# Kernel tuning notes

Hardware: AMD Instinct MI355X
Metric: run time of the kernel (lower is better)

The kernel has to match this reference:

```python
import jax, jax.numpy as jnp
import numpy as np

N = 100000      # num nodes
E = 3200000     # num edges
F = 128         # feature dim (in == out, required by final in-place copy)
U = 1000        # num_users


def gcn_conv(x, edge_index, W, b):
    """PyG GCNConv: symmetric-normalized adjacency with self-loops.
    out = D^{-1/2} (A + I) D^{-1/2} X W + b
    """
    xw = x @ W                                   # [N, F]
    src, dst = edge_index[0], edge_index[1]
    # in-degree including the self-loop (+1)
    deg = jax.ops.segment_sum(jnp.ones((E,), x.dtype), dst, num_segments=N) + 1.0
    inv_sqrt = jax.lax.rsqrt(deg)                # [N]
    coef = inv_sqrt[src] * inv_sqrt[dst]         # [E]
    agg = jax.ops.segment_sum(xw[src] * coef[:, None], dst, num_segments=N)
    # self-loop contribution: norm_ii = inv_sqrt[i]^2
    return agg + xw * (inv_sqrt * inv_sqrt)[:, None] + b


def setup_inputs() -> dict:
    key = jax.random.key(0)
    k1, k2, k3, k4, k5, k6 = jax.random.split(key, 6)
    x = jax.random.normal(k1, (N, F), dtype=jnp.float32)
    edge_index = jax.random.randint(k2, (2, E), 0, N, dtype=jnp.int64)
    s = 1.0 / np.sqrt(F)
    W1 = jax.random.normal(k3, (F, F), dtype=jnp.float32) * s
    b1 = jnp.zeros((F,), dtype=jnp.float32)
    W2 = jax.random.normal(k4, (F, F), dtype=jnp.float32) * s
    b2 = jnp.zeros((F,), dtype=jnp.float32)
    return {"x": x, "edge_index": edge_index, "W1": W1, "b1": b1, "W2": W2, "b2": b2}


def reference(x, edge_index, W1, b1, W2, b2):
    # eval mode: dropout(p=0.5, training=False) is identity; detach is a no-op in fwd
    h = jax.nn.elu(gcn_conv(x, edge_index, W1, b1))
    h = jax.nn.elu(gcn_conv(h, edge_index, W2, b2))
    # x[num_users:] = movie_features  -> movie rows restored to original input
    return jnp.concatenate([h[:U], x[U:]], axis=0)
```

## Files before the change

### kernel.cpp

```cpp
#include <hip/hip_runtime.h>


#define F_DIM 128
#define U_USERS 1000
#define SCAN_CHUNK 1024
#define NFCAP 48000
#define NCHUNK 3
#define SBIN 40960
#define SW (SBIN / 2)
#define PSLICE 85
#define XPAD 136
#define BMW 3136
#define SMEM_BYTES (128 * XPAD * 2 + 64 * XPAD * 2)

using f16x8 = __attribute__((ext_vector_type(8))) _Float16;
using f16x2 = __attribute__((ext_vector_type(2))) _Float16;
using f32x4 = __attribute__((ext_vector_type(4))) float;

union H4 { uint2 u2; _Float16 h[4]; };

__global__ __launch_bounds__(1024) void hist_kernel(const int* __restrict__ src,
                                                    const int* __restrict__ dst,
                                                    unsigned int* __restrict__ partial,
                                                    int* __restrict__ fr, int E, int n) {
    __shared__ unsigned int h[SW];
    int tid = threadIdx.x;
    int c = blockIdx.x % NCHUNK;
    int p = blockIdx.x / NCHUNK;
    for (int i = tid; i < SW; i += 1024) h[i] = 0u;
    __syncthreads();

    int lo = c * SBIN;
    int hi = lo + SBIN;
    int len = (E + PSLICE - 1) / PSLICE;
    int base = p * len;
    int end = min(E, base + len);
    int e = base + tid * 4;
    for (; e + 3 < end; e += 4096) {
        int4 dv = *(const int4*)(dst + e);
#pragma unroll
        for (int i = 0; i < 4; ++i) {
            int d = ((const int*)&dv)[i];
            if ((unsigned)d < (unsigned)n) {
                if (d >= lo && d < hi) {
                    int local = d - lo;
                    atomicAdd(&h[local >> 1], 1u << ((local & 1) << 4));
                }
                if (c == 0 && d < U_USERS) {
                    int s = src[e + i];
                    if ((unsigned)s < (unsigned)n) fr[s] = 1;
                }
            }
        }
    }
    for (; e < end; ++e) {
        int d = dst[e];
        if ((unsigned)d < (unsigned)n) {
            if (d >= lo && d < hi) {
                int local = d - lo;
                atomicAdd(&h[local >> 1], 1u << ((local & 1) << 4));
            }
            if (c == 0 && d < U_USERS) {
                int s = src[e];
                if ((unsigned)s < (unsigned)n) fr[s] = 1;
            }
        }
    }
    __syncthreads();
    unsigned int* outp = partial + ((size_t)(c * PSLICE + p)) * SW;
    for (int i = tid; i < SW; i += 1024) outp[i] = h[i];
}

__global__ void reduce_prep_kernel(const unsigned int* __restrict__ partial,
                                   float* __restrict__ inv, int* __restrict__ fr,
                                   int* __restrict__ degF,
                                   unsigned int* __restrict__ bitsG, int n) {
    int t = blockIdx.x * blockDim.x + threadIdx.x;
    if (t >= NCHUNK * SW) return;
    int c = t / SW, w = t % SW;
    unsigned int a0 = 0, a1 = 0;
    const unsigned int* basep = partial + (size_t)c * PSLICE * SW + w;
#pragma unroll 5
    for (int p = 0; p < PSLICE; ++p) {
        unsigned int v = basep[(size_t)p * SW];
        a0 += v & 0xFFFFu;
        a1 += v >> 16;
    }
    int i0 = c * SBIN + 2 * w;
    unsigned int pair = 0u;
#pragma unroll
    for (int k = 0; k < 2; ++k) {
        int i = i0 + k;
        unsigned int dg = k ? a1 : a0;
        if (i < n) {
            inv[i] = rsqrtf((float)dg + 1.0f);
            bool isfr = (i < U_USERS) || (fr[i] != 0);
            if (i < U_USERS) fr[i] = 1;
            degF[i] = isfr ? (int)dg : 0;
            if (isfr) pair |= (1u << k);
        }
    }
    if (pair) atomicOr(&bitsG[i0 >> 5], pair << (i0 & 31));
}

__global__ void scan_reduce2_kernel(const int* __restrict__ dA, const int* __restrict__ dB,
                                    int* __restrict__ pA, int* __restrict__ pB, int n) {
    __shared__ int sdata[256];
    int b = blockIdx.x, t = threadIdx.x;
    int base = b * SCAN_CHUNK;
    int sumA = 0, sumB = 0;
#pragma unroll
    for (int i = 0; i < 4; ++i) {
        int idx = base + t + 256 * i;
        if (idx < n) { sumA += dA[idx]; sumB += dB[idx]; }
    }
    sdata[t] = sumA; __syncthreads();
    for (int s = 128; s > 0; s >>= 1) { if (t < s) sdata[t] += sdata[t + s]; __syncthreads(); }
    if (t == 0) pA[b] = sdata[0];
    __syncthreads();
    sdata[t] = sumB; __syncthreads();
    for (int s = 128; s > 0; s >>= 1) { if (t < s) sdata[t] += sdata[t + s]; __syncthreads(); }
    if (t == 0) pB[b] = sdata[0];
}

__global__ void scan_partials2_kernel(int* __restrict__ pA, int* __restrict__ pB, int nb) {
    int wv = threadIdx.x >> 6, lane = threadIdx.x & 63;
    int* p = wv ? pB : pA;
    int i0 = lane * 2, i1 = lane * 2 + 1;
    int v0 = (i0 < nb) ? p[i0] : 0;
    int v1 = (i1 < nb) ? p[i1] : 0;
    int sum = v0 + v1;
    int incl = sum;
    for (int ofs = 1; ofs < 64; ofs <<= 1) {
        int t = __shfl_up(incl, ofs);
        if (lane >= ofs) incl += t;
    }
    int run = incl - sum;
    if (i0 < nb) p[i0] = run;
    if (i1 < nb) p[i1] = run + v0;
}

__global__ void scan_final2_kernel(const int* __restrict__ dA, const int* __restrict__ pA,
                                   int* __restrict__ rp,
                                   const int* __restrict__ dB, const int* __restrict__ pB,
                                   int* __restrict__ remap,
                                   int* __restrict__ flist, int* __restrict__ nf_dev, int n) {
    __shared__ int sthread[256];
    int b = blockIdx.x, t = threadIdx.x;
    int base = b * SCAN_CHUNK;
    {
        int v[4]; int sum = 0;
#pragma unroll
        for (int i = 0; i < 4; ++i) { int idx = base + 4 * t + i; v[i] = (idx < n) ? dA[idx] : 0; sum += v[i]; }
        sthread[t] = sum; __syncthreads();
        for (int ofs = 1; ofs < 256; ofs <<= 1) {
            int val = (t >= ofs) ? sthread[t - ofs] : 0;
            __syncthreads(); sthread[t] += val; __syncthreads();
        }
        int run = sthread[t] - sum + pA[b];
#pragma unroll
        for (int i = 0; i < 4; ++i) { int idx = base + 4 * t + i; if (idx < n) rp[idx] = run; run += v[i]; }
        __syncthreads();
    }
    {
        int v[4]; int sum = 0;
#pragma unroll
        for (int i = 0; i < 4; ++i) { int idx = base + 4 * t + i; v[i] = (idx < n) ? dB[idx] : 0; sum += v[i]; }
        sthread[t] = sum; __syncthreads();
        for (int ofs = 1; ofs < 256; ofs <<= 1) {
            int val = (t >= ofs) ? sthread[t - ofs] : 0;
            __syncthreads(); sthread[t] += val; __syncthreads();
        }
        int run = sthread[t] - sum + pB[b];
#pragma unroll
        for (int i = 0; i < 4; ++i) {
            int idx = base + 4 * t + i;
            if (idx < n) {
                remap[idx] = run;
                if (v[i] && run < NFCAP) flist[run] = idx;
                if (idx == n - 1) *nf_dev = min(run + v[i], NFCAP);
            }
            run += v[i];
        }
    }
}

__device__ __forceinline__ void fill_csr_body(const int* __restrict__ src,
                                              const int* __restrict__ dst,
                                              const unsigned int* __restrict__ bitsG,
                                              int* __restrict__ rp, int* __restrict__ col,
                                              int E, int n, int fblk,
                                              unsigned char* smem) {
    unsigned int* bm = (unsigned int*)smem;
    int tid = threadIdx.x;
    int nw = (n + 31) >> 5;
    for (int i = tid; i < nw; i += 256) bm[i] = bitsG[i];
    __syncthreads();

    int t = fblk * 256 + tid;
    int e0 = t * 4;
    if (e0 + 3 < E) {
        int4 dv = *(const int4*)(dst + e0);
        int4 sv = *(const int4*)(src + e0);
        const int* dp = (const int*)&dv;
        const int* sp = (const int*)&sv;
        bool f[4];
#pragma unroll
        for (int i = 0; i < 4; ++i) {
            int d = dp[i];
            f[i] = ((unsigned)d < (unsigned)n) && ((unsigned)sp[i] < (unsigned)n)
                   && ((bm[d >> 5] >> (d & 31)) & 1u);
        }
        int pos[4];
#pragma unroll
        for (int i = 0; i < 4; ++i) {
            pos[i] = -1;
            if (f[i]) pos[i] = atomicAdd(&rp[dp[i]], 1);
        }
#pragma unroll
        for (int i = 0; i < 4; ++i) {
            if (f[i] && (unsigned)pos[i] < (unsigned)E) col[pos[i]] = sp[i];
        }
    } else {
        for (int e = e0; e < E; ++e) {
            int d = dst[e], s = src[e];
            if ((unsigned)d < (unsigned)n && (unsigned)s < (unsigned)n &&
                ((bm[d >> 5] >> (d & 31)) & 1u)) {
                int pos = atomicAdd(&rp[d], 1);
                if ((unsigned)pos < (unsigned)E) col[pos] = s;
            }
        }
    }
}

__device__ __forceinline__ void gemm_mfma_body(const float* __restrict__ X,
                                               const float* __restrict__ W,
                                               _Float16* __restrict__ outh,
                                               float* __restrict__ pout,
                                               int nrows, int rowBase,
                                               unsigned char* smem) {
    _Float16* Wt = (_Float16*)smem;
    _Float16* Xs = Wt + 128 * XPAD;

    int tid = threadIdx.x;

    const float4* W4 = (const float4*)W;
#pragma unroll
    for (int i = 0; i < 16; ++i) {
        int j = tid + 256 * i;
        int k = j >> 5;
        int n4 = j & 31;
        float4 v = W4[j];
#pragma unroll
        for (int q = 0; q < 4; ++q)
            Wt[(n4 * 4 + q) * XPAD + k] = (_Float16)((const float*)&v)[q];
    }

#pragma unroll
    for (int i = 0; i < 8; ++i) {
        int j = tid + 256 * i;
        int r = j >> 5;
        int k4 = j & 31;
        int row = rowBase + r;
        float4 v = make_float4(0.f, 0.f, 0.f, 0.f);
        if (row < nrows) {
            v = ((const float4*)(X + (size_t)row * F_DIM))[k4];
            if (pout != nullptr && row >= U_USERS)
                ((float4*)(pout + (size_t)row * F_DIM))[k4] = v;
        }
        H4 p;
#pragma unroll
        for (int q = 0; q < 4; ++q) p.h[q] = (_Float16)((const float*)&v)[q];
        *(uint2*)&Xs[r * XPAD + k4 * 4] = p.u2;
    }
    __syncthreads();

    int w = tid >> 6;
    int lane = tid & 63;
    int m = lane & 15;
    int quad = lane >> 4;
    int R = w * 16;

    f32x4 acc[8];
#pragma unroll
    for (int i = 0; i < 8; ++i) acc[i] = (f32x4){0.f, 0.f, 0.f, 0.f};

#pragma unroll
    for (int kc = 0; kc < 4; ++kc) {
        f16x8 a = *(const f16x8*)&Xs[(R + m) * XPAD + kc * 32 + quad * 8];
#pragma unroll
        for (int ct = 0; ct < 8; ++ct) {
            f16x8 b = *(const f16x8*)&Wt[(ct * 16 + m) * XPAD + kc * 32 + quad * 8];
            acc[ct] = __builtin_amdgcn_mfma_f32_16x16x32_f16(a, b, acc[ct], 0, 0, 0);
        }
    }

#pragma unroll
    for (int ct = 0; ct < 8; ++ct) {
#pragma unroll
        for (int reg = 0; reg < 4; ++reg) {
            int row = rowBase + R + quad * 4 + reg;
            if (row < nrows)
                outh[(size_t)row * F_DIM + ct * 16 + m] = (_Float16)acc[ct][reg];
        }
    }
}

__global__ __launch_bounds__(256) void gemm_fill_kernel(const float* __restrict__ X,
                                                        const float* __restrict__ W,
                                                        _Float16* __restrict__ outh,
                                                        float* __restrict__ pout, int nrows,
                                                        int gemmBlocks,
                                                        const int* __restrict__ src,
                                                        const int* __restrict__ dst,
                                                        const unsigned int* __restrict__ bitsG,
                                                        int* __restrict__ rp,
                                                        int* __restrict__ col, int E, int n) {
    __shared__ __align__(16) unsigned char smem[SMEM_BYTES];
    int b = blockIdx.x;
    if (b < gemmBlocks) {
        gemm_mfma_body(X, W, outh, pout, nrows, b * 64, smem);
    } else {
        fill_csr_body(src, dst, bitsG, rp, col, E, n, b - gemmBlocks, smem);
    }
}

__global__ __launch_bounds__(256) void gemm_f16_dyn_kernel(const float* __restrict__ X,
                                                           const float* __restrict__ W,
                                                           _Float16* __restrict__ outh,
                                                           const int* __restrict__ nrows_p) {
    __shared__ __align__(16) unsigned char smem[SMEM_BYTES];
    int nrows = *nrows_p;
    int rowBase = blockIdx.x * 64;
    if (rowBase >= nrows) return;
    gemm_mfma_body(X, W, outh, nullptr, nrows, rowBase, smem);
}

__global__ __launch_bounds__(256) void gather_l1_kernel(const _Float16* __restrict__ xwh,
                                                        const float* __restrict__ inv,
                                                        const int* __restrict__ rp,
                                                        const int* __restrict__ col,
                                                        const int* __restrict__ flist,
                                                        const int* __restrict__ nf_p,
                                                        const float* __restrict__ b,
                                                        float* __restrict__ h1c) {
    int ci = blockIdx.x * 4 + (threadIdx.x >> 6);
    if (ci >= *nf_p) return;
    int lane = threadIdx.x & 63;
    int node = flist[ci];
    int start = (node == 0) ? 0 : rp[node - 1];
    int end = rp[node];

    float accx = 0.f, accy = 0.f;
    for (int base = start; base < end; base += 64) {
        int j = base + lane;
        int s_l = 0; float c_l = 0.f;
        if (j < end) { s_l = col[j]; c_l = inv[s_l]; }
        int cnt = min(64, end - base);
        int i = 0;
        for (; i + 4 <= cnt; i += 4) {
            int s0 = __shfl(s_l, i + 0); float f0 = __shfl(c_l, i + 0);
            int s1 = __shfl(s_l, i + 1); float f1 = __shfl(c_l, i + 1);
            int s2 = __shfl(s_l, i + 2); float f2 = __shfl(c_l, i + 2);
            int s3 = __shfl(s_l, i + 3); float f3 = __shfl(c_l, i + 3);
            f16x2 v0 = ((const f16x2*)(xwh + (size_t)s0 * F_DIM))[lane];
            f16x2 v1 = ((const f16x2*)(xwh + (size_t)s1 * F_DIM))[lane];
            f16x2 v2 = ((const f16x2*)(xwh + (size_t)s2 * F_DIM))[lane];
            f16x2 v3 = ((const f16x2*)(xwh + (size_t)s3 * F_DIM))[lane];
            accx += (float)v0[0] * f0 + (float)v1[0] * f1 + (float)v2[0] * f2 + (float)v3[0] * f3;
            accy += (float)v0[1] * f0 + (float)v1[1] * f1 + (float)v2[1] * f2 + (float)v3[1] * f3;
        }
        for (; i < cnt; ++i) {
            int s0 = __shfl(s_l, i); float f0 = __shfl(c_l, i);
            f16x2 v0 = ((const f16x2*)(xwh + (size_t)s0 * F_DIM))[lane];
            accx += (float)v0[0] * f0;
            accy += (float)v0[1] * f0;
        }
    }

    float ivd = inv[node];
    f16x2 self = ((const f16x2*)(xwh + (size_t)node * F_DIM))[lane];
    float vx = accx * ivd + (float)self[0] * ivd * ivd + b[lane * 2];
    float vy = accy * ivd + (float)self[1] * ivd * ivd + b[lane * 2 + 1];
    vx = vx > 0.f ? vx : expf(vx) - 1.f;
    vy = vy > 0.f ? vy : expf(vy) - 1.f;
    ((float2*)(h1c + (size_t)ci * F_DIM))[lane] = make_float2(vx, vy);
}

__global__ __launch_bounds__(256) void gather_l2_kernel(const _Float16* __restrict__ xwc,
                                                        const float* __restrict__ inv,
                                                        const int* __restrict__ rp,
                                                        const int* __restrict__ col,
                                                        const int* __restrict__ remap,
                                                        const float* __restrict__ b,
                                                        float* __restrict__ out) {
    int node = blockIdx.x * 4 + (threadIdx.x >> 6);
    if (node >= U_USERS) return;
    int lane = threadIdx.x & 63;
    int start = (node == 0) ? 0 : rp[node - 1];
    int end = rp[node];

    float accx = 0.f, accy = 0.f;
    for (int base = start; base < end; base += 64) {
        int j = base + lane;
        int r_l = 0; float c_l = 0.f;
        if (j < end) { int s = col[j]; c_l = inv[s]; r_l = remap[s]; }
        int cnt = min(64, end - base);
        int i = 0;
        for (; i + 4 <= cnt; i += 4) {
            int r0 = __shfl(r_l, i + 0); float f0 = __shfl(c_l, i + 0);
            int r1 = __shfl(r_l, i + 1); float f1 = __shfl(c_l, i + 1);
            int r2 = __shfl(r_l, i + 2); float f2 = __shfl(c_l, i + 2);
            int r3 = __shfl(r_l, i + 3); float f3 = __shfl(c_l, i + 3);
            f16x2 v0 = ((const f16x2*)(xwc + (size_t)r0 * F_DIM))[lane];
            f16x2 v1 = ((const f16x2*)(xwc + (size_t)r1 * F_DIM))[lane];
            f16x2 v2 = ((const f16x2*)(xwc + (size_t)r2 * F_DIM))[lane];
            f16x2 v3 = ((const f16x2*)(xwc + (size_t)r3 * F_DIM))[lane];
            accx += (float)v0[0] * f0 + (float)v1[0] * f1 + (float)v2[0] * f2 + (float)v3[0] * f3;
            accy += (float)v0[1] * f0 + (float)v1[1] * f1 + (float)v2[1] * f2 + (float)v3[1] * f3;
        }
        for (; i < cnt; ++i) {
            int rr = __shfl(r_l, i); float f0 = __shfl(c_l, i);
            f16x2 v0 = ((const f16x2*)(xwc + (size_t)rr * F_DIM))[lane];
            accx += (float)v0[0] * f0;
            accy += (float)v0[1] * f0;
        }
    }

    float ivd = inv[node];
    f16x2 self = ((const f16x2*)(xwc + (size_t)node * F_DIM))[lane];
    float vx = accx * ivd + (float)self[0] * ivd * ivd + b[lane * 2];
    float vy = accy * ivd + (float)self[1] * ivd * ivd + b[lane * 2 + 1];
    vx = vx > 0.f ? vx : expf(vx) - 1.f;
    vy = vy > 0.f ? vy : expf(vy) - 1.f;
    ((float2*)(out + (size_t)node * F_DIM))[lane] = make_float2(vx, vy);
}

extern "C" void kernel_launch(void* const* d_in, const int* in_sizes, int n_in,
                              void* d_out, int out_size, void* d_ws, size_t ws_size,
                              hipStream_t stream) {
    const float* x  = (const float*)d_in[0];
    const int*   ei = (const int*)d_in[1];
    const float* W1 = (const float*)d_in[2];
    const float* b1 = (const float*)d_in[3];
    const float* W2 = (const float*)d_in[4];
    const float* b2 = (const float*)d_in[5];
    float* out = (float*)d_out;

    int n = in_sizes[0] / F_DIM;
    int E = in_sizes[1] / 2;
    const int* srcI = ei;
    const int* dstI = ei + E;

    _Float16* xwh = (_Float16*)d_ws;
    float* h1c   = (float*)(xwh + (size_t)n * F_DIM);
    float* inv   = h1c + (size_t)NFCAP * F_DIM;
    int* fr      = (int*)(inv + n);
    int* degF    = fr + n;
    int* remap   = degF + n;
    int* rp      = remap + n;
    int* flist   = rp + n;
    int* pA      = flist + NFCAP;
    int* pB      = pA + 1024;
    int* nf_dev  = pB + 1024;
    int* col     = nf_dev + 16;
    unsigned int* partialH = (unsigned int*)(col + E);
    unsigned int* bitsG = partialH + (size_t)NCHUNK * PSLICE * SW;

    int nb = (n + SCAN_CHUNK - 1) / SCAN_CHUNK;

    hipMemsetAsync(fr, 0, (size_t)n * sizeof(int), stream);
    hipMemsetAsync(bitsG, 0, (size_t)BMW * sizeof(unsigned int), stream);

    hist_kernel<<<NCHUNK * PSLICE, 1024, 0, stream>>>(srcI, dstI, partialH, fr, E, n);
    reduce_prep_kernel<<<(NCHUNK * SW + 255) / 256, 256, 0, stream>>>(partialH, inv, fr, degF, bitsG, n);

    scan_reduce2_kernel<<<nb, 256, 0, stream>>>(degF, fr, pA, pB, n);
    scan_partials2_kernel<<<1, 128, 0, stream>>>(pA, pB, nb);
    scan_final2_kernel<<<nb, 256, 0, stream>>>(degF, pA, rp, fr, pB, remap, flist, nf_dev, n);

    int gemmBlocks = (n + 63) / 64;
    int fillBlocks = (E / 4 + 255) / 256;
    gemm_fill_kernel<<<gemmBlocks + fillBlocks, 256, 0, stream>>>(
        x, W1, xwh, out, n, gemmBlocks, srcI, dstI, bitsG, rp, col, E, n);

    gather_l1_kernel<<<(NFCAP + 3) / 4, 256, 0, stream>>>(xwh, inv, rp, col, flist, nf_dev, b1, h1c);

    gemm_f16_dyn_kernel<<<(NFCAP + 63) / 64, 256, 0, stream>>>(h1c, W2, xwh, nf_dev);
    gather_l2_kernel<<<(U_USERS + 3) / 4, 256, 0, stream>>>(xwh, inv, rp, col, remap, b2, out);
}
```

Baseline: 299.1 us.

## Pre-transpose weights to fp16 once and read B fragments from global

Adds a small kernel that converts and transposes W1 and W2 to fp16 once per call. The GEMM bodies then load MFMA B operands directly from global/L2 instead of each block staging a transposed W copy in LDS, which removes the per-block W conversion and shrinks shared memory to the X tile, allowing higher occupancy. The fused kernel also reorders blocks so the CSR fill blocks are dispatched before the GEMM blocks. The cost is one extra launch, and B reads now come from cache rather than LDS with less reuse per block.

```diff
diff --git a/kernel.cpp b/kernel.cpp
--- a/kernel.cpp
+++ b/kernel.cpp
@@ -11,13 +11,24 @@
 #define PSLICE 85
 #define XPAD 136
 #define BMW 3136
-#define SMEM_BYTES (128 * XPAD * 2 + 64 * XPAD * 2)
+#define SMEM_BYTES (64 * XPAD * 2)
 
 using f16x8 = __attribute__((ext_vector_type(8))) _Float16;
 using f16x2 = __attribute__((ext_vector_type(2))) _Float16;
 using f32x4 = __attribute__((ext_vector_type(4))) float;
 
 union H4 { uint2 u2; _Float16 h[4]; };
+
+__global__ __launch_bounds__(128) void wprep_kernel(const float* __restrict__ W1,
+                                                    const float* __restrict__ W2,
+                                                    _Float16* __restrict__ wt1,
+                                                    _Float16* __restrict__ wt2) {
+    int nr = blockIdx.x & 127;
+    const float* W = (blockIdx.x < 128) ? W1 : W2;
+    _Float16* o = (blockIdx.x < 128) ? wt1 : wt2;
+    int k = threadIdx.x;
+    o[nr * 128 + k] = (_Float16)W[k * 128 + nr];
+}
 
 __global__ __launch_bounds__(1024) void hist_kernel(const int* __restrict__ src,
                                                     const int* __restrict__ dst,
@@ -234,27 +245,13 @@
 }
 
 __device__ __forceinline__ void gemm_mfma_body(const float* __restrict__ X,
-                                               const float* __restrict__ W,
+                                               const _Float16* __restrict__ wth,
                                                _Float16* __restrict__ outh,
                                                float* __restrict__ pout,
                                                int nrows, int rowBase,
                                                unsigned char* smem) {
-    _Float16* Wt = (_Float16*)smem;
-    _Float16* Xs = Wt + 128 * XPAD;
-
+    _Float16* Xs = (_Float16*)smem;
     int tid = threadIdx.x;
-
-    const float4* W4 = (const float4*)W;
-#pragma unroll
-    for (int i = 0; i < 16; ++i) {
-        int j = tid + 256 * i;
-        int k = j >> 5;
-        int n4 = j & 31;
-        float4 v = W4[j];
-#pragma unroll
-        for (int q = 0; q < 4; ++q)
-            Wt[(n4 * 4 + q) * XPAD + k] = (_Float16)((const float*)&v)[q];
-    }
 
 #pragma unroll
     for (int i = 0; i < 8; ++i) {
@@ -290,7 +287,7 @@
         f16x8 a = *(const f16x8*)&Xs[(R + m) * XPAD + kc * 32 + quad * 8];
 #pragma unroll
         for (int ct = 0; ct < 8; ++ct) {
-            f16x8 b = *(const f16x8*)&Wt[(ct * 16 + m) * XPAD + kc * 32 + quad * 8];
+            f16x8 b = *(const f16x8*)&wth[(size_t)(ct * 16 + m) * F_DIM + kc * 32 + quad * 8];
             acc[ct] = __builtin_amdgcn_mfma_f32_16x16x32_f16(a, b, acc[ct], 0, 0, 0);
         }
     }
@@ -307,10 +304,10 @@
 }
 
 __global__ __launch_bounds__(256) void gemm_fill_kernel(const float* __restrict__ X,
-                                                        const float* __restrict__ W,
+                                                        const _Float16* __restrict__ wth,
                                                         _Float16* __restrict__ outh,
                                                         float* __restrict__ pout, int nrows,
-                                                        int gemmBlocks,
+                                                        int fillBlocks,
                                                         const int* __restrict__ src,
                                                         const int* __restrict__ dst,
                                                         const unsigned int* __restrict__ bitsG,
@@ -318,22 +315,22 @@
                                                         int* __restrict__ col, int E, int n) {
     __shared__ __align__(16) unsigned char smem[SMEM_BYTES];
     int b = blockIdx.x;
-    if (b < gemmBlocks) {
-        gemm_mfma_body(X, W, outh, pout, nrows, b * 64, smem);
+    if (b < fillBlocks) {
+        fill_csr_body(src, dst, bitsG, rp, col, E, n, b, smem);
     } else {
-        fill_csr_body(src, dst, bitsG, rp, col, E, n, b - gemmBlocks, smem);
+        gemm_mfma_body(X, wth, outh, pout, nrows, (b - fillBlocks) * 64, smem);
     }
 }
 
 __global__ __launch_bounds__(256) void gemm_f16_dyn_kernel(const float* __restrict__ X,
-                                                           const float* __restrict__ W,
+                                                           const _Float16* __restrict__ wth,
                                                            _Float16* __restrict__ outh,
                                                            const int* __restrict__ nrows_p) {
     __shared__ __align__(16) unsigned char smem[SMEM_BYTES];
     int nrows = *nrows_p;
     int rowBase = blockIdx.x * 64;
     if (rowBase >= nrows) return;
-    gemm_mfma_body(X, W, outh, nullptr, nrows, rowBase, smem);
+    gemm_mfma_body(X, wth, outh, nullptr, nrows, rowBase, smem);
 }
 
 __global__ __launch_bounds__(256) void gather_l1_kernel(const _Float16* __restrict__ xwh,
@@ -466,11 +463,15 @@
     int* col     = nf_dev + 16;
     unsigned int* partialH = (unsigned int*)(col + E);
     unsigned int* bitsG = partialH + (size_t)NCHUNK * PSLICE * SW;
+    _Float16* wt1h = (_Float16*)(bitsG + BMW);
+    _Float16* wt2h = wt1h + 16384;
 
     int nb = (n + SCAN_CHUNK - 1) / SCAN_CHUNK;
 
     hipMemsetAsync(fr, 0, (size_t)n * sizeof(int), stream);
     hipMemsetAsync(bitsG, 0, (size_t)BMW * sizeof(unsigned int), stream);
+
+    wprep_kernel<<<256, 128, 0, stream>>>(W1, W2, wt1h, wt2h);
 
     hist_kernel<<<NCHUNK * PSLICE, 1024, 0, stream>>>(srcI, dstI, partialH, fr, E, n);
     reduce_prep_kernel<<<(NCHUNK * SW + 255) / 256, 256, 0, stream>>>(partialH, inv, fr, degF, bitsG, n);
@@ -479,13 +480,13 @@
     scan_partials2_kernel<<<1, 128, 0, stream>>>(pA, pB, nb);
     scan_final2_kernel<<<nb, 256, 0, stream>>>(degF, pA, rp, fr, pB, remap, flist, nf_dev, n);
 
+    int fillBlocks = (E / 4 + 255) / 256;
     int gemmBlocks = (n + 63) / 64;
-    int fillBlocks = (E / 4 + 255) / 256;
-    gemm_fill_kernel<<<gemmBlocks + fillBlocks, 256, 0, stream>>>(
-        x, W1, xwh, out, n, gemmBlocks, srcI, dstI, bitsG, rp, col, E, n);
+    gemm_fill_kernel<<<fillBlocks + gemmBlocks, 256, 0, stream>>>(
+        x, wt1h, xwh, out, n, fillBlocks, srcI, dstI, bitsG, rp, col, E, n);
 
     gather_l1_kernel<<<(NFCAP + 3) / 4, 256, 0, stream>>>(xwh, inv, rp, col, flist, nf_dev, b1, h1c);
 
-    gemm_f16_dyn_kernel<<<(NFCAP + 63) / 64, 256, 0, stream>>>(h1c, W2, xwh, nf_dev);
+    gemm_f16_dyn_kernel<<<(NFCAP + 63) / 64, 256, 0, stream>>>(h1c, wt2h, xwh, nf_dev);
     gather_l2_kernel<<<(U_USERS + 3) / 4, 256, 0, stream>>>(xwh, inv, rp, col, remap, b2, out);
 }
```

After: 309.8 us. 1.04x slower.

## Load GEMM A operands straight to registers and swizzle W tile in LDS

Applied to the files above, without the earlier changes.

The MFMA GEMM no longer stages X rows through shared memory. Each lane loads its A fragments directly from global memory into registers and converts them to f16. The transposed W tile is stored unpadded with an XOR swizzle to avoid bank conflicts, which cuts LDS use to 32KB. The fused kernel also puts the fill-CSR blocks before the GEMM blocks so that the scatter work starts first. The trade-off is less coalesced global reads of X and strided per-element reads of W.

```diff
diff --git a/kernel.cpp b/kernel.cpp
--- a/kernel.cpp
+++ b/kernel.cpp
@@ -11,13 +11,11 @@
 #define PSLICE 85
 #define XPAD 136
 #define BMW 3136
-#define SMEM_BYTES (128 * XPAD * 2 + 64 * XPAD * 2)
+#define SMEM_BYTES 32768
 
 using f16x8 = __attribute__((ext_vector_type(8))) _Float16;
 using f16x2 = __attribute__((ext_vector_type(2))) _Float16;
 using f32x4 = __attribute__((ext_vector_type(4))) float;
-
-union H4 { uint2 u2; _Float16 h[4]; };
 
 __global__ __launch_bounds__(1024) void hist_kernel(const int* __restrict__ src,
                                                     const int* __restrict__ dst,
@@ -240,38 +238,18 @@
                                                int nrows, int rowBase,
                                                unsigned char* smem) {
     _Float16* Wt = (_Float16*)smem;
-    _Float16* Xs = Wt + 128 * XPAD;
-
     int tid = threadIdx.x;
-
-    const float4* W4 = (const float4*)W;
-#pragma unroll
-    for (int i = 0; i < 16; ++i) {
-        int j = tid + 256 * i;
-        int k = j >> 5;
-        int n4 = j & 31;
-        float4 v = W4[j];
-#pragma unroll
-        for (int q = 0; q < 4; ++q)
-            Wt[(n4 * 4 + q) * XPAD + k] = (_Float16)((const float*)&v)[q];
-    }
 
 #pragma unroll
     for (int i = 0; i < 8; ++i) {
         int j = tid + 256 * i;
-        int r = j >> 5;
-        int k4 = j & 31;
-        int row = rowBase + r;
-        float4 v = make_float4(0.f, 0.f, 0.f, 0.f);
-        if (row < nrows) {
-            v = ((const float4*)(X + (size_t)row * F_DIM))[k4];
-            if (pout != nullptr && row >= U_USERS)
-                ((float4*)(pout + (size_t)row * F_DIM))[k4] = v;
-        }
-        H4 p;
-#pragma unroll
-        for (int q = 0; q < 4; ++q) p.h[q] = (_Float16)((const float*)&v)[q];
-        *(uint2*)&Xs[r * XPAD + k4 * 4] = p.u2;
+        int nr = j & 127;
+        int k8 = j >> 7;
+        f16x8 v;
+#pragma unroll
+        for (int kk = 0; kk < 8; ++kk)
+            v[kk] = (_Float16)W[(k8 * 8 + kk) * F_DIM + nr];
+        *(f16x8*)&Wt[nr * F_DIM + ((k8 ^ (nr & 15)) * 8)] = v;
     }
     __syncthreads();
 
@@ -279,7 +257,35 @@
     int lane = tid & 63;
     int m = lane & 15;
     int quad = lane >> 4;
-    int R = w * 16;
+    int row = rowBase + w * 16 + m;
+    bool rv = row < nrows;
+
+    f16x8 a0, a1, a2, a3;
+    {
+        const float* xr = X + (size_t)row * F_DIM;
+        float* pr = (pout != nullptr && rv && row >= U_USERS)
+                        ? pout + (size_t)row * F_DIM : nullptr;
+#pragma unroll
+        for (int kc = 0; kc < 4; ++kc) {
+            float4 lo = make_float4(0.f, 0.f, 0.f, 0.f);
+            float4 hi = lo;
+            if (rv) {
+                lo = ((const float4*)(xr + kc * 32 + quad * 8))[0];
+                hi = ((const float4*)(xr + kc * 32 + quad * 8))[1];
+            }
+            if (pr) {
+                ((float4*)(pr + kc * 32 + quad * 8))[0] = lo;
+                ((float4*)(pr + kc * 32 + quad * 8))[1] = hi;
+            }
+            f16x8 av;
+            av[0] = (_Float16)lo.x; av[1] = (_Float16)lo.y;
+            av[2] = (_Float16)lo.z; av[3] = (_Float16)lo.w;
+            av[4] = (_Float16)hi.x; av[5] = (_Float16)hi.y;
+            av[6] = (_Float16)hi.z; av[7] = (_Float16)hi.w;
+            if (kc == 0) a0 = av; else if (kc == 1) a1 = av;
+            else if (kc == 2) a2 = av; else a3 = av;
+        }
+    }
 
     f32x4 acc[8];
 #pragma unroll
@@ -287,10 +293,11 @@
 
 #pragma unroll
     for (int kc = 0; kc < 4; ++kc) {
-        f16x8 a = *(const f16x8*)&Xs[(R + m) * XPAD + kc * 32 + quad * 8];
+        f16x8 a = (kc == 0) ? a0 : (kc == 1) ? a1 : (kc == 2) ? a2 : a3;
 #pragma unroll
         for (int ct = 0; ct < 8; ++ct) {
-            f16x8 b = *(const f16x8*)&Wt[(ct * 16 + m) * XPAD + kc * 32 + quad * 8];
+            f16x8 b = *(const f16x8*)&Wt[(ct * 16 + m) * F_DIM +
+                                         (((kc * 4 + quad) ^ m) * 8)];
             acc[ct] = __builtin_amdgcn_mfma_f32_16x16x32_f16(a, b, acc[ct], 0, 0, 0);
         }
     }
@@ -299,9 +306,9 @@
     for (int ct = 0; ct < 8; ++ct) {
 #pragma unroll
         for (int reg = 0; reg < 4; ++reg) {
-            int row = rowBase + R + quad * 4 + reg;
-            if (row < nrows)
-                outh[(size_t)row * F_DIM + ct * 16 + m] = (_Float16)acc[ct][reg];
+            int r = rowBase + w * 16 + quad * 4 + reg;
+            if (r < nrows)
+                outh[(size_t)r * F_DIM + ct * 16 + m] = (_Float16)acc[ct][reg];
         }
     }
 }
@@ -310,7 +317,7 @@
                                                         const float* __restrict__ W,
                                                         _Float16* __restrict__ outh,
                                                         float* __restrict__ pout, int nrows,
-                                                        int gemmBlocks,
+                                                        int fillBlocks,
                                                         const int* __restrict__ src,
                                                         const int* __restrict__ dst,
                                                         const unsigned int* __restrict__ bitsG,
@@ -318,10 +325,10 @@
                                                         int* __restrict__ col, int E, int n) {
     __shared__ __align__(16) unsigned char smem[SMEM_BYTES];
     int b = blockIdx.x;
-    if (b < gemmBlocks) {
-        gemm_mfma_body(X, W, outh, pout, nrows, b * 64, smem);
+    if (b < fillBlocks) {
+        fill_csr_body(src, dst, bitsG, rp, col, E, n, b, smem);
     } else {
-        fill_csr_body(src, dst, bitsG, rp, col, E, n, b - gemmBlocks, smem);
+        gemm_mfma_body(X, W, outh, pout, nrows, (b - fillBlocks) * 64, smem);
     }
 }
 
@@ -479,10 +486,10 @@
     scan_partials2_kernel<<<1, 128, 0, stream>>>(pA, pB, nb);
     scan_final2_kernel<<<nb, 256, 0, stream>>>(degF, pA, rp, fr, pB, remap, flist, nf_dev, n);
 
+    int fillBlocks = (E / 4 + 255) / 256;
     int gemmBlocks = (n + 63) / 64;
-    int fillBlocks = (E / 4 + 255) / 256;
-    gemm_fill_kernel<<<gemmBlocks + fillBlocks, 256, 0, stream>>>(
-        x, W1, xwh, out, n, gemmBlocks, srcI, dstI, bitsG, rp, col, E, n);
+    gemm_fill_kernel<<<fillBlocks + gemmBlocks, 256, 0, stream>>>(
+        x, W1, xwh, out, n, fillBlocks, srcI, dstI, bitsG, rp, col, E, n);
 
     gather_l1_kernel<<<(NFCAP + 3) / 4, 256, 0, stream>>>(xwh, inv, rp, col, flist, nf_dev, b1, h1c);
 
```

New measurement: 296.9 us. About the same (-0.7%).
